# Performance work log

Hardware: AMD Instinct MI355X
Metric: run time of the kernel (lower is better)

Reference implementation:

```python
import jax, jax.numpy as jnp
import numpy as np

NUM_HEADS = 16
HIDDEN = 1024
HEADSIZE = HIDDEN // NUM_HEADS


def setup_inputs() -> dict:
    key = jax.random.key(0)
    ks = jax.random.split(key, 9)
    B, S, H = 4, 2048, HIDDEN
    s = 1.0 / np.sqrt(H)
    return {
        "x": jax.random.normal(ks[0], (B, S, H), dtype=jnp.float32),
        "Wq": jax.random.normal(ks[1], (H, H), dtype=jnp.float32) * s,
        "bq": jax.random.normal(ks[2], (H,), dtype=jnp.float32) * s,
        "Wk": jax.random.normal(ks[3], (H, H), dtype=jnp.float32) * s,
        "bk": jax.random.normal(ks[4], (H,), dtype=jnp.float32) * s,
        "Wv": jax.random.normal(ks[5], (H, H), dtype=jnp.float32) * s,
        "bv": jax.random.normal(ks[6], (H,), dtype=jnp.float32) * s,
        "Wo": jax.random.normal(ks[7], (H, H), dtype=jnp.float32) * s,
        "bo": jax.random.normal(ks[8], (H,), dtype=jnp.float32) * s,
    }


def reference(x, Wq, bq, Wk, bk, Wv, bv, Wo, bo):
    B, S, H = x.shape
    nh, hs = NUM_HEADS, HEADSIZE

    def split_heads(y):  # (B,S,H) -> (B,nh,S,hs)
        return y.reshape(B, S, nh, hs).transpose(0, 2, 1, 3)

    q = split_heads(x @ Wq.T + bq)
    k = split_heads(x @ Wk.T + bk)
    v = split_heads(x @ Wv.T + bv)

    scores = jnp.einsum("bhqd,bhkd->bhqk", q, k) / jnp.sqrt(jnp.float32(hs))
    # causal mask: q_ind < k_ind gets -1e9 (matches torch.where(mask, -1e9, scores))
    q_ind = jnp.arange(S)[:, None]
    k_ind = jnp.arange(S)[None, :]
    scores = jnp.where(q_ind < k_ind, jnp.float32(-1e9), scores)
    attn = jax.nn.softmax(scores, axis=-1)
    out = jnp.einsum("bhqk,bhkd->bhqd", attn, v)  # (B,nh,S,hs)
    out = out.transpose(0, 2, 1, 3).reshape(B, S, H)
    return out @ Wo.T + bo
```

## Files before the change

kernel.cpp:

```cpp
#include <hip/hip_runtime.h>

#define NH 16
#define HS 64
#define HID 1024
#define SEQ 2048
#define BB 4
#define MR (BB*SEQ)
#define KD 1024
#define NT 32
#define QSCALE 0.18033688f

typedef __bf16 bf16;
typedef __attribute__((ext_vector_type(8))) __bf16 bf16x8;
typedef __attribute__((ext_vector_type(4))) __bf16 bf16x4;
typedef __attribute__((ext_vector_type(4))) float f32x4;
typedef __attribute__((ext_vector_type(16))) float f32x16;
typedef __attribute__((ext_vector_type(4))) float f4;
typedef __attribute__((ext_vector_type(2))) unsigned uintx2;

typedef __attribute__((address_space(3))) unsigned int as3u;
typedef __attribute__((address_space(1))) unsigned int as1u;

__device__ __forceinline__ void gl_lds16(const void* g, void* l) {
  __builtin_amdgcn_global_load_lds((const as1u*)g, (as3u*)l, 16, 0, 0);
}

__device__ __forceinline__ f32x4 mfma16(bf16x8 a, bf16x8 b, f32x4 c) {
  return __builtin_amdgcn_mfma_f32_16x16x32_bf16(a, b, c, 0, 0, 0);
}

__device__ __forceinline__ f32x16 mfma32(bf16x8 a, bf16x8 b, f32x16 c) {
  return __builtin_amdgcn_mfma_f32_32x32x16_bf16(a, b, c, 0, 0, 0);
}

__device__ __forceinline__ uintx2 plswap(unsigned a, unsigned b) {
#if __has_builtin(__builtin_amdgcn_permlane32_swap)
  return __builtin_amdgcn_permlane32_swap(a, b, false, false);
#else
  asm volatile("v_permlane32_swap_b32 %0, %1" : "+&v"(a), "+v"(b));
  uintx2 r; r[0] = a; r[1] = b; return r;
#endif
}

__device__ __forceinline__ float xmax32(float x) {
  uintx2 r = plswap(__float_as_uint(x), __float_as_uint(x));
  return fmaxf(__uint_as_float(r[0]), __uint_as_float(r[1]));
}
__device__ __forceinline__ float xadd32(float x) {
  uintx2 r = plswap(__float_as_uint(x), __float_as_uint(x));
  return __uint_as_float(r[0]) + __uint_as_float(r[1]);
}

__device__ __forceinline__ unsigned cvtpk(float lo, float hi) {
  unsigned r;
  asm("v_cvt_pk_bf16_f32 %0, %1, %2" : "=v"(r) : "v"(lo), "v"(hi));
  return r;
}

__global__ __launch_bounds__(256) void k_cvt(const float* __restrict__ in,
                                             bf16* __restrict__ out, int n4) {
  int i = blockIdx.x * 256 + threadIdx.x;
  if (i >= n4) return;
  f4 v = reinterpret_cast<const f4*>(in)[i];
  bf16x4 h;
  h[0] = (bf16)v[0]; h[1] = (bf16)v[1]; h[2] = (bf16)v[2]; h[3] = (bf16)v[3];
  reinterpret_cast<bf16x4*>(out)[i] = h;
}

__global__ __launch_bounds__(256) void k_cvt4(const float* __restrict__ w0, const float* __restrict__ w1,
                                              const float* __restrict__ w2, const float* __restrict__ w3,
                                              bf16* __restrict__ o0, bf16* __restrict__ o1,
                                              bf16* __restrict__ o2, bf16* __restrict__ o3, int n4) {
  int i = blockIdx.x * 256 + threadIdx.x;
  if (i >= n4) return;
  const float* in = (blockIdx.y == 0) ? w0 : (blockIdx.y == 1) ? w1 : (blockIdx.y == 2) ? w2 : w3;
  bf16* out = (blockIdx.y == 0) ? o0 : (blockIdx.y == 1) ? o1 : (blockIdx.y == 2) ? o2 : o3;
  f4 v = reinterpret_cast<const f4*>(in)[i];
  bf16x4 h;
  h[0] = (bf16)v[0]; h[1] = (bf16)v[1]; h[2] = (bf16)v[2]; h[3] = (bf16)v[3];
  reinterpret_cast<bf16x4*>(out)[i] = h;
}

template<int MODE>
__global__ __launch_bounds__(512, 4) void k_gemm_p(const bf16* __restrict__ A,
                                                   const bf16* __restrict__ w0, const bf16* __restrict__ w1,
                                                   const bf16* __restrict__ w2,
                                                   const float* __restrict__ b0, const float* __restrict__ b1,
                                                   const float* __restrict__ b2p,
                                                   void* __restrict__ o0, void* __restrict__ o1,
                                                   void* __restrict__ o2) {
  __shared__ __align__(16) bf16 As[3][128*32];
  __shared__ __align__(16) bf16 Bs[3][256*32];
  const int tid = threadIdx.x, l = tid & 63, w = tid >> 6;
  const int wr = w >> 2, wc = w & 3;
  const int m0 = blockIdx.x * 128;
  const int ny = blockIdx.y;
  const int which = (MODE == 0) ? (ny >> 2) : 0;
  const int n0 = (MODE == 0) ? (ny & 3) * 256 : ny * 256;
  const bf16* Bw = (MODE == 1) ? w0 : (which == 0 ? w0 : which == 1 ? w1 : w2);
  const float* bias = (MODE == 1) ? b0 : (which == 0 ? b0 : which == 1 ? b1 : b2p);

  const int sra = tid >> 2;
  const int sca = (tid & 3) ^ ((sra >> 1) & 3);
  const bf16* Ag = A  + (size_t)(m0 + sra) * KD + sca * 8;
  const bf16* Bg = Bw + (size_t)(n0 + sra) * KD + sca * 8;

  gl_lds16(Ag,                        (char*)As[0] + w * 1024);
  gl_lds16(Bg,                        (char*)Bs[0] + w * 1024);
  gl_lds16(Bg + (size_t)128 * KD,     (char*)Bs[0] + 8192 + w * 1024);
  gl_lds16(Ag + 32,                   (char*)As[1] + w * 1024);
  gl_lds16(Bg + 32,                   (char*)Bs[1] + w * 1024);
  gl_lds16(Bg + (size_t)128 * KD + 32, (char*)Bs[1] + 8192 + w * 1024);

  f32x4 acc[4][4] = {};

  const int la = l & 15, lg = l >> 4;

  for (int t = 0; t < NT; ++t) {
    const int bq = t % 3;
    if (t < NT - 1) { asm volatile("s_waitcnt vmcnt(3)" ::: "memory"); }
    else            { asm volatile("s_waitcnt vmcnt(0)" ::: "memory"); }
    __builtin_amdgcn_sched_barrier(0);
    __builtin_amdgcn_s_barrier();
    __builtin_amdgcn_sched_barrier(0);

    bf16x8 af[4], bf_[2];
    #pragma unroll
    for (int mf = 0; mf < 4; mf++) {
      const int ra = wr * 64 + mf * 16 + la;
      const int ca = lg ^ ((ra >> 1) & 3);
      af[mf] = *(const bf16x8*)((const char*)As[bq] + ra * 64 + ca * 16);
    }
    #pragma unroll
    for (int nf = 0; nf < 2; nf++) {
      const int rb = wc * 64 + nf * 16 + la;
      const int cb = lg ^ ((rb >> 1) & 3);
      bf_[nf] = *(const bf16x8*)((const char*)Bs[bq] + rb * 64 + cb * 16);
    }
    const int t2 = t + 2;
    if (t2 < NT) {
      const int b2 = t2 % 3;
      gl_lds16(Ag + t2 * 32, (char*)As[b2] + w * 1024);
      gl_lds16(Bg + t2 * 32, (char*)Bs[b2] + w * 1024);
    }
    asm volatile("s_waitcnt lgkmcnt(0)" ::: "memory");
    __builtin_amdgcn_sched_barrier(0);
    __builtin_amdgcn_s_setprio(1);
    #pragma unroll
    for (int mf = 0; mf < 4; mf++) {
      acc[mf][0] = mfma16(af[mf], bf_[0], acc[mf][0]);
      acc[mf][1] = mfma16(af[mf], bf_[1], acc[mf][1]);
    }
    __builtin_amdgcn_s_setprio(0);

    #pragma unroll
    for (int nf = 0; nf < 2; nf++) {
      const int rb = wc * 64 + (nf + 2) * 16 + la;
      const int cb = lg ^ ((rb >> 1) & 3);
      bf_[nf] = *(const bf16x8*)((const char*)Bs[bq] + rb * 64 + cb * 16);
    }
    if (t2 < NT) {
      const int b2 = t2 % 3;
      gl_lds16(Bg + (size_t)128 * KD + t2 * 32, (char*)Bs[b2] + 8192 + w * 1024);
    }
    asm volatile("s_waitcnt lgkmcnt(0)" ::: "memory");
    __builtin_amdgcn_sched_barrier(0);
    __builtin_amdgcn_s_setprio(1);
    #pragma unroll
    for (int mf = 0; mf < 4; mf++) {
      acc[mf][2] = mfma16(af[mf], bf_[0], acc[mf][2]);
      acc[mf][3] = mfma16(af[mf], bf_[1], acc[mf][3]);
    }
    __builtin_amdgcn_s_setprio(0);
  }

  const float scale = (MODE == 0 && which == 0) ? QSCALE : 1.0f;
  #pragma unroll
  for (int mf = 0; mf < 4; mf++) {
    #pragma unroll
    for (int nf = 0; nf < 4; nf++) {
      const int n = n0 + wc * 64 + nf * 16 + la;
      const float bn = bias[n];
      #pragma unroll
      for (int j = 0; j < 4; j++) {
        const int m = m0 + wr * 64 + mf * 16 + lg * 4 + j;
        const float v = (acc[mf][nf][j] + bn) * scale;
        if (MODE == 0) {
          if (which == 2) {
            ((bf16*)o2)[(((size_t)(m >> 11) * NH + (n >> 6)) * HS + (n & 63)) * SEQ + (m & (SEQ - 1))] = (bf16)v;
          } else {
            bf16* dst = (which == 0) ? (bf16*)o0 : (bf16*)o1;
            dst[(((size_t)(m >> 11) * NH + (n >> 6)) * SEQ + (m & (SEQ - 1))) * HS + (n & 63)] = (bf16)v;
          }
        } else {
          ((float*)o0)[(size_t)m * HID + n] = v;
        }
      }
    }
  }
}

__global__ __launch_bounds__(256, 2) void k_attn(const bf16* __restrict__ Q,
                                                 const bf16* __restrict__ K,
                                                 const bf16* __restrict__ Vt,
                                                 bf16* __restrict__ Aout) {
  const int bh = blockIdx.y;
  const int bx = blockIdx.x;
  const int tid = threadIdx.x, l = tid & 63, w = tid >> 6;
  const int hi = l >> 5;

  __shared__ __align__(16) bf16 Qs[128*64];
  __shared__ __align__(16) bf16 Ks[2][64*64];
  __shared__ __align__(16) bf16 Vs[2][64*64];

  const bf16* Qg = Q  + (size_t)bh * SEQ * HS;
  const bf16* Kg = K  + (size_t)bh * SEQ * HS;
  const bf16* Vg = Vt + (size_t)bh * HS * SEQ;

  const int bb = bh >> 4, hh = bh & 15;
  const int sr  = tid >> 3;
  const int swz = ((tid & 7) ^ (sr & 7)) * 8;

  for (int pass = 0; pass < 2; ++pass) {
    const int p_ = pass ? (15 - bx) : bx;
    const int q0 = p_ * 128;
    const int nt = 2 * p_ + 2;

    __syncthreads();

    #pragma unroll
    for (int i = 0; i < 4; i++)
      gl_lds16(Qg + (size_t)(q0 + 32*i + sr) * HS + swz, (char*)Qs + i*4096 + w*1024);
    #pragma unroll
    for (int i = 0; i < 2; i++) {
      gl_lds16(Kg + (size_t)(32*i + sr) * HS + swz,  (char*)Ks[0] + i*4096 + w*1024);
      gl_lds16(Vg + (size_t)(32*i + sr) * SEQ + swz, (char*)Vs[0] + i*4096 + w*1024);
    }
    __syncthreads();

    bf16x8 qf[4];
    {
      const int qrow = w*32 + (l & 31);
      #pragma unroll
      for (int m = 0; m < 4; m++) {
        const int cc = 2*m + hi;
        qf[m] = *(const bf16x8*)((const char*)Qs + qrow*128 + ((cc ^ (qrow & 7))*16));
      }
    }

    float m_r = -1e30f, l_r = 0.f;
    f32x16 o[2] = {};
    const int qmax = q0 + w*32 + 31;
    const int qg   = q0 + w*32 + (l & 31);

    int cur = 0;
    for (int kt = 0; kt < nt; ++kt) {
      const int k0 = kt * 64;

      if (kt + 1 < nt) {
        const int k1 = k0 + 64;
        #pragma unroll
        for (int i = 0; i < 2; i++) {
          gl_lds16(Kg + (size_t)(k1 + 32*i + sr) * HS + swz,  (char*)Ks[cur^1] + i*4096 + w*1024);
          gl_lds16(Vg + (size_t)(32*i + sr) * SEQ + k1 + swz, (char*)Vs[cur^1] + i*4096 + w*1024);
        }
      }

      if (k0 <= qmax) {
        f32x16 p[2] = {};
        #pragma unroll
        for (int b = 0; b < 2; b++) {
          #pragma unroll
          for (int m = 0; m < 4; m++) {
            const int row = 32*b + (l & 31);
            const int cc = 2*m + hi;
            bf16x8 kf = *(const bf16x8*)((const char*)Ks[cur] + row*128 + ((cc ^ (row & 7))*16));
            p[b] = mfma32(kf, qf[m], p[b]);
          }
        }

        if (k0 + 63 > q0 + w*32) {
          #pragma unroll
          for (int b = 0; b < 2; b++)
            #pragma unroll
            for (int r = 0; r < 16; r++) {
              const int kg = k0 + 32*b + (r & 3) + 8*(r >> 2) + 4*hi;
              if (kg > qg) p[b][r] = -1e30f;
            }
        }

        float rloc = -1e30f;
        #pragma unroll
        for (int b = 0; b < 2; b++)
          #pragma unroll
          for (int r = 0; r < 16; r++) rloc = fmaxf(rloc, p[b][r]);
        const float rmax = xmax32(rloc);

        if (__any(rmax > m_r + 8.0f)) {
          const float mn = fmaxf(m_r, rmax);
          const float alpha = __builtin_amdgcn_exp2f(m_r - mn);
          m_r = mn;
          l_r *= alpha;
          #pragma unroll
          for (int r = 0; r < 16; r++) {
            const float ar = __shfl(alpha, (r & 3) + 8*(r >> 2) + 4*hi);
            o[0][r] *= ar; o[1][r] *= ar;
          }
        }

        float sloc = 0.f;
        #pragma unroll
        for (int b = 0; b < 2; b++)
          #pragma unroll
          for (int r = 0; r < 16; r++) {
            const float e = __builtin_amdgcn_exp2f(p[b][r] - m_r);
            p[b][r] = e;
            sloc += e;
          }
        l_r += xadd32(sloc);

        bf16x8 pa[4];
        #pragma unroll
        for (int c = 0; c < 4; c++) {
          const int b = c >> 1, R = (c & 1) * 8;
          unsigned w01 = cvtpk(p[b][R+0], p[b][R+1]);
          unsigned w23 = cvtpk(p[b][R+2], p[b][R+3]);
          unsigned w89 = cvtpk(p[b][R+4], p[b][R+5]);
          unsigned wab = cvtpk(p[b][R+6], p[b][R+7]);
          uintx2 s1 = plswap(w01, w89);
          uintx2 s2 = plswap(w23, wab);
          union { unsigned u[4]; bf16x8 v; } uu;
          uu.u[0] = s1[0]; uu.u[1] = s2[0]; uu.u[2] = s1[1]; uu.u[3] = s2[1];
          pa[c] = uu.v;
        }

        #pragma unroll
        for (int d = 0; d < 2; d++) {
          #pragma unroll
          for (int c = 0; c < 4; c++) {
            const int row = 32*d + (l & 31);
            const int cc = 2*c + hi;
            bf16x8 vf = *(const bf16x8*)((const char*)Vs[cur] + row*128 + ((cc ^ (row & 7))*16));
            o[d] = mfma32(pa[c], vf, o[d]);
          }
        }
      }

      __syncthreads();
      cur ^= 1;
    }

    const float inv = 1.0f / l_r;
    #pragma unroll
    for (int r = 0; r < 16; r++) {
      const int qr = (r & 3) + 8*(r >> 2) + 4*hi;
      const float ir = __shfl(inv, qr);
      const int q = q0 + w*32 + qr;
      #pragma unroll
      for (int d = 0; d < 2; d++)
        Aout[(size_t)(bb*SEQ + q)*HID + hh*HS + d*32 + (l & 31)] = (bf16)(o[d][r] * ir);
    }
  }
}

extern "C" void kernel_launch(void* const* d_in, const int* in_sizes, int n_in,
                              void* d_out, int out_size, void* d_ws, size_t ws_size,
                              hipStream_t stream) {
  const float* x  = (const float*)d_in[0];
  const float* Wq = (const float*)d_in[1];
  const float* bq = (const float*)d_in[2];
  const float* Wk = (const float*)d_in[3];
  const float* bk = (const float*)d_in[4];
  const float* Wv = (const float*)d_in[5];
  const float* bv = (const float*)d_in[6];
  const float* Wo = (const float*)d_in[7];
  const float* bo = (const float*)d_in[8];

  char* ws = (char*)d_ws;
  const size_t MB = 1024 * 1024;
  bf16* xb  = (bf16*)(ws);
  bf16* wqb = (bf16*)(ws + 16*MB);
  bf16* wkb = (bf16*)(ws + 18*MB);
  bf16* wvb = (bf16*)(ws + 20*MB);
  bf16* wob = (bf16*)(ws + 22*MB);
  bf16* Qb  = (bf16*)(ws + 24*MB);
  bf16* Kb  = (bf16*)(ws + 40*MB);
  bf16* Vb  = (bf16*)(ws + 56*MB);
  bf16* Ab  = xb;

  k_cvt<<<MR*HID/4/256, 256, 0, stream>>>(x, xb, MR*HID/4);
  k_cvt4<<<dim3(HID*KD/4/256, 4), 256, 0, stream>>>(Wq, Wk, Wv, Wo, wqb, wkb, wvb, wob, HID*KD/4);

  k_gemm_p<0><<<dim3(MR/128, 12), 512, 0, stream>>>(xb, wqb, wkb, wvb, bq, bk, bv, Qb, Kb, Vb);

  k_attn<<<dim3(8, BB*NH), 256, 0, stream>>>(Qb, Kb, Vb, Ab);

  k_gemm_p<1><<<dim3(MR/128, 4), 512, 0, stream>>>(Ab, wob, wob, wob, bo, bo, bo, d_out, d_out, d_out);
}
```

Before: 170.7 us.

## Triple-buffer K/V in attention, load Q directly to registers, fuse convert kernels

The attention kernel moves from double to triple-buffered K/V tiles with a prefetch distance of two, and replaces the __syncthreads with an explicit vmcnt wait plus a barrier. Q fragments are now read straight from global memory into registers, which removes the Q LDS staging buffer and cuts LDS use so three blocks can target each CU. The attention grid is transposed so consecutive blocks cover different heads. The two fp32-to-bf16 conversion kernels are merged into one launch. In exchange, the vmcnt counting has to stay exact, and the direct Q loads are less coalesced.

```diff
diff --git a/kernel.cpp b/kernel.cpp
--- a/kernel.cpp
+++ b/kernel.cpp
@@ -57,28 +57,25 @@
   return r;
 }
 
-__global__ __launch_bounds__(256) void k_cvt(const float* __restrict__ in,
-                                             bf16* __restrict__ out, int n4) {
+#define XN4   (MR*HID/4)
+#define WN4   (HID*KD/4)
+__global__ __launch_bounds__(256) void k_cvt_all(const float* __restrict__ x,
+                                                 const float* __restrict__ w0, const float* __restrict__ w1,
+                                                 const float* __restrict__ w2, const float* __restrict__ w3,
+                                                 bf16* __restrict__ xb,
+                                                 bf16* __restrict__ o0, bf16* __restrict__ o1,
+                                                 bf16* __restrict__ o2, bf16* __restrict__ o3) {
   int i = blockIdx.x * 256 + threadIdx.x;
-  if (i >= n4) return;
-  f4 v = reinterpret_cast<const f4*>(in)[i];
+  const float* in; bf16* out; int j;
+  if (i < XN4)            { in = x;  out = xb; j = i; }
+  else if (i < XN4+WN4)   { in = w0; out = o0; j = i - XN4; }
+  else if (i < XN4+2*WN4) { in = w1; out = o1; j = i - XN4 - WN4; }
+  else if (i < XN4+3*WN4) { in = w2; out = o2; j = i - XN4 - 2*WN4; }
+  else                    { in = w3; out = o3; j = i - XN4 - 3*WN4; }
+  f4 v = reinterpret_cast<const f4*>(in)[j];
   bf16x4 h;
   h[0] = (bf16)v[0]; h[1] = (bf16)v[1]; h[2] = (bf16)v[2]; h[3] = (bf16)v[3];
-  reinterpret_cast<bf16x4*>(out)[i] = h;
-}
-
-__global__ __launch_bounds__(256) void k_cvt4(const float* __restrict__ w0, const float* __restrict__ w1,
-                                              const float* __restrict__ w2, const float* __restrict__ w3,
-                                              bf16* __restrict__ o0, bf16* __restrict__ o1,
-                                              bf16* __restrict__ o2, bf16* __restrict__ o3, int n4) {
-  int i = blockIdx.x * 256 + threadIdx.x;
-  if (i >= n4) return;
-  const float* in = (blockIdx.y == 0) ? w0 : (blockIdx.y == 1) ? w1 : (blockIdx.y == 2) ? w2 : w3;
-  bf16* out = (blockIdx.y == 0) ? o0 : (blockIdx.y == 1) ? o1 : (blockIdx.y == 2) ? o2 : o3;
-  f4 v = reinterpret_cast<const f4*>(in)[i];
-  bf16x4 h;
-  h[0] = (bf16)v[0]; h[1] = (bf16)v[1]; h[2] = (bf16)v[2]; h[3] = (bf16)v[3];
-  reinterpret_cast<bf16x4*>(out)[i] = h;
+  reinterpret_cast<bf16x4*>(out)[j] = h;
 }
 
 template<int MODE>
@@ -113,7 +110,6 @@
   gl_lds16(Bg + (size_t)128 * KD + 32, (char*)Bs[1] + 8192 + w * 1024);
 
   f32x4 acc[4][4] = {};
-
   const int la = l & 15, lg = l >> 4;
 
   for (int t = 0; t < NT; ++t) {
@@ -200,18 +196,17 @@
   }
 }
 
-__global__ __launch_bounds__(256, 2) void k_attn(const bf16* __restrict__ Q,
+__global__ __launch_bounds__(256, 3) void k_attn(const bf16* __restrict__ Q,
                                                  const bf16* __restrict__ K,
                                                  const bf16* __restrict__ Vt,
                                                  bf16* __restrict__ Aout) {
-  const int bh = blockIdx.y;
-  const int bx = blockIdx.x;
+  const int bh = blockIdx.x;
+  const int bx = blockIdx.y;
   const int tid = threadIdx.x, l = tid & 63, w = tid >> 6;
   const int hi = l >> 5;
 
-  __shared__ __align__(16) bf16 Qs[128*64];
-  __shared__ __align__(16) bf16 Ks[2][64*64];
-  __shared__ __align__(16) bf16 Vs[2][64*64];
+  __shared__ __align__(16) bf16 Ks[3][64*64];
+  __shared__ __align__(16) bf16 Vs[3][64*64];
 
   const bf16* Qg = Q  + (size_t)bh * SEQ * HS;
   const bf16* Kg = K  + (size_t)bh * SEQ * HS;
@@ -226,27 +221,29 @@
     const int q0 = p_ * 128;
     const int nt = 2 * p_ + 2;
 
-    __syncthreads();
-
-    #pragma unroll
-    for (int i = 0; i < 4; i++)
-      gl_lds16(Qg + (size_t)(q0 + 32*i + sr) * HS + swz, (char*)Qs + i*4096 + w*1024);
+    bf16x8 qf[4];
+    {
+      const bf16* qrow = Qg + (size_t)(q0 + w*32 + (l & 31)) * HS + hi * 8;
+      #pragma unroll
+      for (int m = 0; m < 4; m++)
+        qf[m] = *(const bf16x8*)(qrow + m * 16);
+    }
+    __builtin_amdgcn_sched_barrier(0);
+
     #pragma unroll
     for (int i = 0; i < 2; i++) {
       gl_lds16(Kg + (size_t)(32*i + sr) * HS + swz,  (char*)Ks[0] + i*4096 + w*1024);
       gl_lds16(Vg + (size_t)(32*i + sr) * SEQ + swz, (char*)Vs[0] + i*4096 + w*1024);
     }
-    __syncthreads();
-
-    bf16x8 qf[4];
-    {
-      const int qrow = w*32 + (l & 31);
-      #pragma unroll
-      for (int m = 0; m < 4; m++) {
-        const int cc = 2*m + hi;
-        qf[m] = *(const bf16x8*)((const char*)Qs + qrow*128 + ((cc ^ (qrow & 7))*16));
-      }
-    }
+    #pragma unroll
+    for (int i = 0; i < 2; i++) {
+      gl_lds16(Kg + (size_t)(64 + 32*i + sr) * HS + swz,  (char*)Ks[1] + i*4096 + w*1024);
+      gl_lds16(Vg + (size_t)(32*i + sr) * SEQ + 64 + swz, (char*)Vs[1] + i*4096 + w*1024);
+    }
+    asm volatile("s_waitcnt vmcnt(4)" ::: "memory");
+    __builtin_amdgcn_sched_barrier(0);
+    __builtin_amdgcn_s_barrier();
+    __builtin_amdgcn_sched_barrier(0);
 
     float m_r = -1e30f, l_r = 0.f;
     f32x16 o[2] = {};
@@ -257,12 +254,13 @@
     for (int kt = 0; kt < nt; ++kt) {
       const int k0 = kt * 64;
 
-      if (kt + 1 < nt) {
-        const int k1 = k0 + 64;
+      if (kt + 2 < nt) {
+        const int k2 = k0 + 128;
+        const int b2 = (cur == 0) ? 2 : cur - 1;
         #pragma unroll
         for (int i = 0; i < 2; i++) {
-          gl_lds16(Kg + (size_t)(k1 + 32*i + sr) * HS + swz,  (char*)Ks[cur^1] + i*4096 + w*1024);
-          gl_lds16(Vg + (size_t)(32*i + sr) * SEQ + k1 + swz, (char*)Vs[cur^1] + i*4096 + w*1024);
+          gl_lds16(Kg + (size_t)(k2 + 32*i + sr) * HS + swz,  (char*)Ks[b2] + i*4096 + w*1024);
+          gl_lds16(Vg + (size_t)(32*i + sr) * SEQ + k2 + swz, (char*)Vs[b2] + i*4096 + w*1024);
         }
       }
 
@@ -346,8 +344,12 @@
         }
       }
 
-      __syncthreads();
-      cur ^= 1;
+      if (kt + 2 < nt) { asm volatile("s_waitcnt vmcnt(4)" ::: "memory"); }
+      else             { asm volatile("s_waitcnt vmcnt(0)" ::: "memory"); }
+      __builtin_amdgcn_sched_barrier(0);
+      __builtin_amdgcn_s_barrier();
+      __builtin_amdgcn_sched_barrier(0);
+      cur = (cur == 2) ? 0 : cur + 1;
     }
 
     const float inv = 1.0f / l_r;
@@ -388,12 +390,11 @@
   bf16* Vb  = (bf16*)(ws + 56*MB);
   bf16* Ab  = xb;
 
-  k_cvt<<<MR*HID/4/256, 256, 0, stream>>>(x, xb, MR*HID/4);
-  k_cvt4<<<dim3(HID*KD/4/256, 4), 256, 0, stream>>>(Wq, Wk, Wv, Wo, wqb, wkb, wvb, wob, HID*KD/4);
+  k_cvt_all<<<(XN4 + 4*WN4 + 255)/256, 256, 0, stream>>>(x, Wq, Wk, Wv, Wo, xb, wqb, wkb, wvb, wob);
 
   k_gemm_p<0><<<dim3(MR/128, 12), 512, 0, stream>>>(xb, wqb, wkb, wvb, bq, bk, bv, Qb, Kb, Vb);
 
-  k_attn<<<dim3(8, BB*NH), 256, 0, stream>>>(Qb, Kb, Vb, Ab);
+  k_attn<<<dim3(BB*NH, 8), 256, 0, stream>>>(Qb, Kb, Vb, Ab);
 
   k_gemm_p<1><<<dim3(MR/128, 4), 512, 0, stream>>>(Ab, wob, wob, wob, bo, bo, bo, d_out, d_out, d_out);
 }
```

Measured after the change: 170.8 us (median of 2 runs). About the same (+0.1%).
